# Kernel tuning notes

Hardware: AMD Instinct MI355X
Metric: run time of the kernel (lower is better)

Reference implementation:

```python
import jax, jax.numpy as jnp
import numpy as np

D, E, H, B, K = 2, 16, 1024, 8192, 2  # depth, experts, width, tokens, selection_size


def setup_inputs() -> dict:
    key = jax.random.key(0)
    ks = jax.random.split(key, 6)
    X = jax.random.normal(ks[0], (B, H), dtype=jnp.float32)
    # gate Linear per layer (torch inits these to zero; small random used so top-k is nontrivial)
    gate_w = jax.random.normal(ks[1], (D, E, H), dtype=jnp.float32) * 0.02
    gate_b = jnp.zeros((D, E), dtype=jnp.float32)
    # per-expert Linear: weight [out,in], bias [out], stacked over (layer, expert)
    ew = jax.random.normal(ks[2], (D, E, H, H), dtype=jnp.float32) * (1.0 / np.float32(np.sqrt(H)))
    eb = jnp.zeros((D, E, H), dtype=jnp.float32)
    # PReLU params: left/right slopes ~ randn (as in torch init), position/bias zero
    pl = jax.random.normal(ks[3], (D, E, H), dtype=jnp.float32)
    pr = jax.random.normal(ks[4], (D, E, H), dtype=jnp.float32)
    pp = jnp.zeros((D, E, H), dtype=jnp.float32)
    pb = jnp.zeros((D, E, H), dtype=jnp.float32)
    return {"X": X, "gate_w": gate_w, "gate_b": gate_b, "ew": ew, "eb": eb,
            "pl": pl, "pr": pr, "pp": pp, "pb": pb}


def reference(X, gate_w, gate_b, ew, eb, pl, pr, pp, pb):
    x = X
    for d in range(D):  # small fixed layer loop
        # gating: Linear -> top-k -> softmax over selected logits
        G = jnp.einsum('bi,ei->be', x, gate_w[d]) + gate_b[d]          # [B,E]
        vals, idx = jax.lax.top_k(G, K)                                 # [B,K]
        w = jax.nn.softmax(vals, axis=-1)                               # [B,K]
        # expert Linear over all experts, then custom PReLU
        y = jnp.einsum('bi,eoi->beo', x, ew[d]) + eb[d]                 # [B,E,O]
        delta = y - pp[d]                                               # [B,E,O]
        act = pb[d] + jnp.where(delta >= 0, delta * pr[d], delta * pl[d])
        # gather selected experts and combine
        sel = jnp.take_along_axis(act, idx[:, :, None], axis=1)        # [B,K,O]
        x = jnp.einsum('bk,bko->bo', w, sel)                            # [B,O]
    return x
```

## Files before the change

kernel.cpp:

```cpp
#include <hip/hip_runtime.h>

#define H_ 1024
#define B_ 8192
#define E_ 16
#define D_ 2
#define BM 128
#define BN 128
#define BK 32

typedef _Float16 f16;
typedef _Float16 f16x4 __attribute__((ext_vector_type(4)));
typedef _Float16 f16x8 __attribute__((ext_vector_type(8)));
typedef float    f32x4 __attribute__((ext_vector_type(4)));

__device__ __forceinline__ void gload16(const void* g, void* l) {
  __builtin_amdgcn_global_load_lds((const __attribute__((address_space(1))) void*)g,
                                   (__attribute__((address_space(3))) void*)l, 16, 0, 0);
}

__global__ void split_kernel(const float* __restrict__ s, f16* __restrict__ hp,
                             f16* __restrict__ lp, int n) {
  const int stride = gridDim.x * blockDim.x * 4;
  for (int i = (blockIdx.x * blockDim.x + threadIdx.x) * 4; i < n; i += stride) {
    float4 v = *(const float4*)(s + i);
    f16 h0 = (f16)v.x, h1 = (f16)v.y, h2 = (f16)v.z, h3 = (f16)v.w;
    f16 l0 = (f16)(v.x - (float)h0), l1 = (f16)(v.y - (float)h1);
    f16 l2 = (f16)(v.z - (float)h2), l3 = (f16)(v.w - (float)h3);
    *(f16x4*)(hp + i) = (f16x4){h0, h1, h2, h3};
    *(f16x4*)(lp + i) = (f16x4){l0, l1, l2, l3};
  }
}

__global__ void gate_kernel(const float* __restrict__ x, const float* __restrict__ gw,
                            const float* __restrict__ gb, int2* __restrict__ tok_e,
                            float2* __restrict__ tok_w) {
  const int token = blockIdx.x * 4 + (threadIdx.x >> 6);
  const int lane = threadIdx.x & 63;
  const float4* xr = (const float4*)(x + (long)token * H_);
  float acc[E_];
#pragma unroll
  for (int e = 0; e < E_; ++e) acc[e] = 0.f;
#pragma unroll
  for (int i0 = 0; i0 < H_ / 4; i0 += 64) {
    float4 xv = xr[i0 + lane];
#pragma unroll
    for (int e = 0; e < E_; ++e) {
      float4 gv = ((const float4*)(gw + e * H_))[i0 + lane];
      acc[e] = fmaf(xv.x, gv.x, fmaf(xv.y, gv.y, fmaf(xv.z, gv.z, fmaf(xv.w, gv.w, acc[e]))));
    }
  }
#pragma unroll
  for (int off = 32; off; off >>= 1) {
#pragma unroll
    for (int e = 0; e < E_; ++e) acc[e] += __shfl_xor(acc[e], off, 64);
  }
  if (lane == 0) {
    float g[E_];
#pragma unroll
    for (int e = 0; e < E_; ++e) g[e] = acc[e] + gb[e];
    int i0 = 0; float v0 = g[0];
#pragma unroll
    for (int e = 1; e < E_; ++e) if (g[e] > v0) { v0 = g[e]; i0 = e; }
    int i1 = -1; float v1 = -3.4e38f;
#pragma unroll
    for (int e = 0; e < E_; ++e) if (e != i0 && g[e] > v1) { v1 = g[e]; i1 = e; }
    float t = expf(v1 - v0);
    float s = 1.f / (1.f + t);
    tok_e[token] = (int2){i0, i1};
    tok_w[token] = (float2){s, t * s};
  }
}

__global__ void route_kernel(const int2* __restrict__ tok_e, const float2* __restrict__ tok_w,
                             int* __restrict__ lists, float* __restrict__ wlist,
                             int* __restrict__ counts) {
  __shared__ int cnt[E_];
  __shared__ int base[E_];
  const int tid = threadIdx.x;
  const int token = blockIdx.x * 256 + tid;
  if (tid < E_) cnt[tid] = 0;
  __syncthreads();
  int2 e = tok_e[token];
  float2 w = tok_w[token];
  int p0 = atomicAdd(&cnt[e.x], 1);
  int p1 = atomicAdd(&cnt[e.y], 1);
  __syncthreads();
  if (tid < E_) base[tid] = atomicAdd(&counts[tid], cnt[tid]);
  __syncthreads();
  int o0 = e.x * B_ + base[e.x] + p0;
  lists[o0] = token; wlist[o0] = w.x;
  int o1 = e.y * B_ + base[e.y] + p1;
  lists[o1] = token; wlist[o1] = w.y;
}

__global__ __launch_bounds__(256, 2) void expert_gemm(
    const f16* __restrict__ xh, const f16* __restrict__ xl,
    const f16* __restrict__ wh, const f16* __restrict__ wl,
    const float* __restrict__ eb, const float* __restrict__ pl,
    const float* __restrict__ pr, const float* __restrict__ pp,
    const float* __restrict__ pb, const int* __restrict__ lists,
    const float* __restrict__ wlist, const int* __restrict__ counts,
    float* __restrict__ out) {
  const int e = blockIdx.z;
  const int cnt = counts[e];
  const int mt = blockIdx.y;
  if (mt * BM >= cnt) return;
  const int nt = blockIdx.x;

  __shared__ char smem[32768 + BM * 8];
  int* tokS = (int*)(smem + 32768);
  float* wtS = (float*)(smem + 32768 + BM * 4);

  const int tid = threadIdx.x;
  const int lane = tid & 63;
  const int wave = tid >> 6;
  const int wm = wave >> 1, wn = wave & 1;

  if (tid < BM) {
    int gr = mt * BM + tid;
    int tok = 0; float wgt = 0.f;
    if (gr < cnt) { tok = lists[e * B_ + gr]; wgt = wlist[e * B_ + gr]; }
    tokS[tid] = tok; wtS[tid] = wgt;
  }
  __syncthreads();

  const int rl = lane >> 2;
  const int ks = ((lane & 3) - ((lane >> 3) & 3)) & 3;
  const int c0 = wave * 2, c1 = wave * 2 + 1;
  const int rA0 = c0 * 16 + rl, rA1 = c1 * 16 + rl;
  const long a0 = (long)tokS[rA0] * H_ + ks * 8;
  const long a1 = (long)tokS[rA1] * H_ + ks * 8;
  const long b0 = ((long)e * H_ + nt * BN + rA0) * H_ + ks * 8;
  const long b1 = ((long)e * H_ + nt * BN + rA1) * H_ + ks * 8;

  const int rm = lane & 15;
  const int sl = ((((lane >> 4) + (rm >> 1)) & 3) << 4);
  int offA[4], offB[4];
#pragma unroll
  for (int m = 0; m < 4; ++m) offA[m] = (wm * 64 + m * 16 + rm) * 64 + sl;
#pragma unroll
  for (int n = 0; n < 4; ++n) offB[n] = (wn * 64 + n * 16 + rm) * 64 + sl;

  f32x4 acc[4][4] = {};

  for (int kt = 0; kt < H_; kt += BK) {
    gload16(xh + a0 + kt, smem + c0 * 1024);
    gload16(xh + a1 + kt, smem + c1 * 1024);
    gload16(xl + a0 + kt, smem + 8192 + c0 * 1024);
    gload16(xl + a1 + kt, smem + 8192 + c1 * 1024);
    gload16(wh + b0 + kt, smem + 16384 + c0 * 1024);
    gload16(wh + b1 + kt, smem + 16384 + c1 * 1024);
    gload16(wl + b0 + kt, smem + 24576 + c0 * 1024);
    gload16(wl + b1 + kt, smem + 24576 + c1 * 1024);
    __syncthreads();

    f16x8 Amh[4], Aml[4], Bnh[4], Bnl[4];
#pragma unroll
    for (int m = 0; m < 4; ++m) {
      Amh[m] = *(const f16x8*)(smem + offA[m]);
      Aml[m] = *(const f16x8*)(smem + 8192 + offA[m]);
    }
#pragma unroll
    for (int n = 0; n < 4; ++n) {
      Bnh[n] = *(const f16x8*)(smem + 16384 + offB[n]);
      Bnl[n] = *(const f16x8*)(smem + 24576 + offB[n]);
    }
#pragma unroll
    for (int m = 0; m < 4; ++m) {
#pragma unroll
      for (int n = 0; n < 4; ++n) {
        acc[m][n] = __builtin_amdgcn_mfma_f32_16x16x32_f16(Amh[m], Bnh[n], acc[m][n], 0, 0, 0);
        acc[m][n] = __builtin_amdgcn_mfma_f32_16x16x32_f16(Amh[m], Bnl[n], acc[m][n], 0, 0, 0);
        acc[m][n] = __builtin_amdgcn_mfma_f32_16x16x32_f16(Aml[m], Bnh[n], acc[m][n], 0, 0, 0);
      }
    }
    __syncthreads();
  }

  float ebv[4], plv[4], prv[4], ppv[4], pbv[4];
  int Ocol[4];
#pragma unroll
  for (int n = 0; n < 4; ++n) {
    int O = nt * BN + wn * 64 + n * 16 + rm;
    Ocol[n] = O;
    int idx = e * H_ + O;
    ebv[n] = eb[idx]; plv[n] = pl[idx]; prv[n] = pr[idx]; ppv[n] = pp[idx]; pbv[n] = pb[idx];
  }
  const int rbase = (lane >> 4) * 4;
#pragma unroll
  for (int m = 0; m < 4; ++m) {
#pragma unroll
    for (int j = 0; j < 4; ++j) {
      int rloc = wm * 64 + m * 16 + rbase + j;
      int gr = mt * BM + rloc;
      if (gr < cnt) {
        float wgt = wtS[rloc];
        long obase = (long)tokS[rloc] * H_;
#pragma unroll
        for (int n = 0; n < 4; ++n) {
          float y = acc[m][n][j] + ebv[n];
          float dlt = y - ppv[n];
          float act = pbv[n] + (dlt >= 0.f ? dlt * prv[n] : dlt * plv[n]);
          atomicAdd(out + obase + Ocol[n], wgt * act);
        }
      }
    }
  }
}

extern "C" void kernel_launch(void* const* d_in, const int* in_sizes, int n_in,
                              void* d_out, int out_size, void* d_ws, size_t ws_size,
                              hipStream_t stream) {
  const float* X  = (const float*)d_in[0];
  const float* GW = (const float*)d_in[1];
  const float* GB = (const float*)d_in[2];
  const float* EW = (const float*)d_in[3];
  const float* EB = (const float*)d_in[4];
  const float* PL = (const float*)d_in[5];
  const float* PR = (const float*)d_in[6];
  const float* PP = (const float*)d_in[7];
  const float* PB = (const float*)d_in[8];
  float* out = (float*)d_out;

  char* ws = (char*)d_ws;
  float* x1    = (float*)(ws);
  f16*   xh    = (f16*)(ws + 33554432);
  f16*   xl    = (f16*)(ws + 50331648);
  f16*   wh    = (f16*)(ws + 67108864);
  f16*   wl    = (f16*)(ws + 100663296);
  int*   lists = (int*)(ws + 134217728);
  float* wlist = (float*)(ws + 134742016);
  int*   counts= (int*)(ws + 135266304);
  int2*  tok_e = (int2*)(ws + 135266368);
  float2* tok_w= (float2*)(ws + 135331904);

  for (int d = 0; d < D_; ++d) {
    const float* xin = d ? x1 : X;
    float* xout = d ? out : x1;
    hipMemsetAsync(counts, 0, 64, stream);
    hipMemsetAsync(xout, 0, (size_t)B_ * H_ * 4, stream);
    split_kernel<<<2048, 256, 0, stream>>>(xin, xh, xl, B_ * H_);
    split_kernel<<<2048, 256, 0, stream>>>(EW + (size_t)d * E_ * H_ * H_, wh, wl, E_ * H_ * H_);
    gate_kernel<<<B_ / 4, 256, 0, stream>>>(xin, GW + d * E_ * H_, GB + d * E_,
                                            tok_e, tok_w);
    route_kernel<<<B_ / 256, 256, 0, stream>>>(tok_e, tok_w, lists, wlist, counts);
    expert_gemm<<<dim3(H_ / BN, B_ / BM, E_), 256, 0, stream>>>(
        xh, xl, wh, wl, EB + d * E_ * H_, PL + d * E_ * H_, PR + d * E_ * H_,
        PP + d * E_ * H_, PB + d * E_ * H_, lists, wlist, counts, xout);
  }
}
```

Baseline: 638.1 us.

## Fuse activation split into gating, compact expert tile grid, raise occupancy

The fp16 hi/lo split of the activations now happens inside the gate kernel, which removes a separate pass over X. A single-thread build_tiles kernel compacts the (expert, m-tile) pairs, so the expert GEMM launches 144 tile rows instead of 64×16 mostly-empty blocks. The per-block shared token and weight staging is replaced by direct global reads, and launch bounds are raised to 4 blocks per SM. The risks are a serial single-thread launch, more register pressure under the tighter launch bounds, and silently dropped tiles if a routing ever needs more than 144 tiles.

Result: no change. 643.7 us (+0.9%).

```diff
diff --git a/kernel.cpp b/kernel.cpp
--- a/kernel.cpp
+++ b/kernel.cpp
@@ -7,6 +7,7 @@
 #define BM 128
 #define BN 128
 #define BK 32
+#define MAXT 144
 
 typedef _Float16 f16;
 typedef _Float16 f16x4 __attribute__((ext_vector_type(4)));
@@ -31,18 +32,25 @@
   }
 }
 
-__global__ void gate_kernel(const float* __restrict__ x, const float* __restrict__ gw,
-                            const float* __restrict__ gb, int2* __restrict__ tok_e,
-                            float2* __restrict__ tok_w) {
+__global__ void gate_split(const float* __restrict__ x, const float* __restrict__ gw,
+                           const float* __restrict__ gb, f16* __restrict__ xh,
+                           f16* __restrict__ xl, int2* __restrict__ tok_e,
+                           float2* __restrict__ tok_w) {
   const int token = blockIdx.x * 4 + (threadIdx.x >> 6);
   const int lane = threadIdx.x & 63;
   const float4* xr = (const float4*)(x + (long)token * H_);
+  f16x4* hr = (f16x4*)(xh + (long)token * H_);
+  f16x4* lr = (f16x4*)(xl + (long)token * H_);
   float acc[E_];
 #pragma unroll
   for (int e = 0; e < E_; ++e) acc[e] = 0.f;
 #pragma unroll
   for (int i0 = 0; i0 < H_ / 4; i0 += 64) {
     float4 xv = xr[i0 + lane];
+    f16 h0 = (f16)xv.x, h1 = (f16)xv.y, h2 = (f16)xv.z, h3 = (f16)xv.w;
+    hr[i0 + lane] = (f16x4){h0, h1, h2, h3};
+    lr[i0 + lane] = (f16x4){(f16)(xv.x - (float)h0), (f16)(xv.y - (float)h1),
+                            (f16)(xv.z - (float)h2), (f16)(xv.w - (float)h3)};
 #pragma unroll
     for (int e = 0; e < E_; ++e) {
       float4 gv = ((const float4*)(gw + e * H_))[i0 + lane];
@@ -93,43 +101,50 @@
   lists[o1] = token; wlist[o1] = w.y;
 }
 
-__global__ __launch_bounds__(256, 2) void expert_gemm(
+__global__ void build_tiles(const int* __restrict__ counts, int2* __restrict__ tiles,
+                            int* __restrict__ ntile) {
+  if (threadIdx.x == 0) {
+    int n = 0;
+    for (int e = 0; e < E_; ++e) {
+      int c = counts[e];
+      for (int mt = 0; mt * BM < c; ++mt) tiles[n++] = (int2){e, mt};
+    }
+    *ntile = n;
+  }
+}
+
+__global__ __launch_bounds__(256, 4) void expert_gemm(
     const f16* __restrict__ xh, const f16* __restrict__ xl,
     const f16* __restrict__ wh, const f16* __restrict__ wl,
     const float* __restrict__ eb, const float* __restrict__ pl,
     const float* __restrict__ pr, const float* __restrict__ pp,
     const float* __restrict__ pb, const int* __restrict__ lists,
     const float* __restrict__ wlist, const int* __restrict__ counts,
+    const int2* __restrict__ tiles, const int* __restrict__ ntile,
     float* __restrict__ out) {
-  const int e = blockIdx.z;
+  const int t = blockIdx.y;
+  if (t >= *ntile) return;
+  const int2 td = tiles[t];
+  const int e = td.x, mt = td.y;
   const int cnt = counts[e];
-  const int mt = blockIdx.y;
-  if (mt * BM >= cnt) return;
   const int nt = blockIdx.x;
 
-  __shared__ char smem[32768 + BM * 8];
-  int* tokS = (int*)(smem + 32768);
-  float* wtS = (float*)(smem + 32768 + BM * 4);
+  __shared__ char smem[32768];
 
   const int tid = threadIdx.x;
   const int lane = tid & 63;
   const int wave = tid >> 6;
   const int wm = wave >> 1, wn = wave & 1;
 
-  if (tid < BM) {
-    int gr = mt * BM + tid;
-    int tok = 0; float wgt = 0.f;
-    if (gr < cnt) { tok = lists[e * B_ + gr]; wgt = wlist[e * B_ + gr]; }
-    tokS[tid] = tok; wtS[tid] = wgt;
-  }
-  __syncthreads();
-
   const int rl = lane >> 2;
   const int ks = ((lane & 3) - ((lane >> 3) & 3)) & 3;
   const int c0 = wave * 2, c1 = wave * 2 + 1;
   const int rA0 = c0 * 16 + rl, rA1 = c1 * 16 + rl;
-  const long a0 = (long)tokS[rA0] * H_ + ks * 8;
-  const long a1 = (long)tokS[rA1] * H_ + ks * 8;
+  const int gr0 = mt * BM + rA0, gr1 = mt * BM + rA1;
+  const int tok0 = (gr0 < cnt) ? lists[e * B_ + gr0] : 0;
+  const int tok1 = (gr1 < cnt) ? lists[e * B_ + gr1] : 0;
+  const long a0 = (long)tok0 * H_ + ks * 8;
+  const long a1 = (long)tok1 * H_ + ks * 8;
   const long b0 = ((long)e * H_ + nt * BN + rA0) * H_ + ks * 8;
   const long b1 = ((long)e * H_ + nt * BN + rA1) * H_ + ks * 8;
 
@@ -194,8 +209,8 @@
       int rloc = wm * 64 + m * 16 + rbase + j;
       int gr = mt * BM + rloc;
       if (gr < cnt) {
-        float wgt = wtS[rloc];
-        long obase = (long)tokS[rloc] * H_;
+        float wgt = wlist[e * B_ + gr];
+        long obase = (long)lists[e * B_ + gr] * H_;
 #pragma unroll
         for (int n = 0; n < 4; ++n) {
           float y = acc[m][n][j] + ebv[n];
@@ -233,19 +248,21 @@
   int*   counts= (int*)(ws + 135266304);
   int2*  tok_e = (int2*)(ws + 135266368);
   float2* tok_w= (float2*)(ws + 135331904);
+  int2*  tiles = (int2*)(ws + 135397440);
+  int*   ntile = (int*)(ws + 135398592);
 
   for (int d = 0; d < D_; ++d) {
     const float* xin = d ? x1 : X;
     float* xout = d ? out : x1;
     hipMemsetAsync(counts, 0, 64, stream);
     hipMemsetAsync(xout, 0, (size_t)B_ * H_ * 4, stream);
-    split_kernel<<<2048, 256, 0, stream>>>(xin, xh, xl, B_ * H_);
     split_kernel<<<2048, 256, 0, stream>>>(EW + (size_t)d * E_ * H_ * H_, wh, wl, E_ * H_ * H_);
-    gate_kernel<<<B_ / 4, 256, 0, stream>>>(xin, GW + d * E_ * H_, GB + d * E_,
-                                            tok_e, tok_w);
+    gate_split<<<B_ / 4, 256, 0, stream>>>(xin, GW + d * E_ * H_, GB + d * E_,
+                                           xh, xl, tok_e, tok_w);
     route_kernel<<<B_ / 256, 256, 0, stream>>>(tok_e, tok_w, lists, wlist, counts);
-    expert_gemm<<<dim3(H_ / BN, B_ / BM, E_), 256, 0, stream>>>(
+    build_tiles<<<1, 64, 0, stream>>>(counts, tiles, ntile);
+    expert_gemm<<<dim3(H_ / BN, MAXT), 256, 0, stream>>>(
         xh, xl, wh, wl, EB + d * E_ * H_, PL + d * E_ * H_, PR + d * E_ * H_,
-        PP + d * E_ * H_, PB + d * E_ * H_, lists, wlist, counts, xout);
-  }
-}
+        PP + d * E_ * H_, PB + d * E_ * H_, lists, wlist, counts, tiles, ntile, xout);
+  }
+}
```
